# Performance work log

Measured on AMD Instinct MI355X. Metric: run time of the kernel, lower is better.

Reference implementation:

```python
import jax, jax.numpy as jnp
import numpy as np

B, TK, NK, H, E, V = 128, 400, 50, 256, 256, 50000


def setup_inputs() -> dict:
    key = jax.random.key(0)
    ks = iter(jax.random.split(key, 48))
    def rn(shape, s=1.0):
        return jax.random.normal(next(ks), shape, jnp.float32) * s
    def ru(shape):
        return jax.random.uniform(next(ks), shape, jnp.float32)
    z = lambda shape: jnp.zeros(shape, jnp.float32)
    s = 0.05
    inp = {}
    inp['y_t_1'] = jax.random.randint(next(ks), (B,), 0, V)
    inp['h_prev'] = rn((B, H))
    inp['c_prev'] = rn((B, H))
    inp['encoder_outputs'] = rn((B, TK, H))
    inp['encoder_outputs_node'] = rn((B, NK, H))
    inp['enc_padding_mask'] = jnp.ones((B, TK), jnp.float32)
    inp['enc_padding_mask_node'] = jnp.ones((B, NK), jnp.float32)
    inp['c_t_d'] = rn((B, H))
    inp['c_t_g'] = rn((B, H))
    inp['c_t_g2'] = rn((B, H))
    inp['coverage'] = z((B, TK))
    inp['flow'] = ru((B, NK))
    inp['node_to_token'] = ru((B, NK, TK))
    inp['graph'] = ru((B, NK, NK))
    inp['voc_d'] = jax.random.randint(next(ks), (B, TK), 0, V)
    inp['step'] = 0
    # learned parameters
    inp['emb_table'] = rn((V, E), s)
    inp['Wx'] = rn((4 * H, E), s); inp['bx'] = z((E,))
    inp['Wi'] = rn((E, 4 * H), s); inp['Wh'] = rn((H, 4 * H), s)
    inp['bi'] = z((4 * H,)); inp['bh'] = z((4 * H,))
    inp['Whd'] = rn((H, H), s); inp['Wsd'] = rn((2 * H, H), s)
    inp['wcd'] = rn((H,), s); inp['vd'] = rn((H,), s); inp['bd'] = z((H,))
    inp['Wn'] = rn((H, H), s); inp['Wsf'] = rn((2 * H, H), s)
    inp['vf'] = rn((H,), s); inp['bf'] = z((H,))
    inp['Wpg'] = rn((5 * H + E, 1), s); inp['bpg'] = z((1,))
    inp['W1'] = rn((4 * H, H), s); inp['b1'] = z((H,))
    inp['W2'] = rn((H, V), s); inp['b2'] = z((V,))
    return inp


def _forward(y_t_1, h_prev, c_prev, enc, enc_n, mask_t, mask_n, c_t_d, c_t_g, c_t_g2,
             coverage, flow, n2t, graph, voc_d, emb_table, Wx, bx, Wi, Wh, bi, bh,
             Whd, Wsd, wcd, vd, bd, Wn, Wsf, vf, bf, Wpg, bpg, W1, b1, W2, b2):
    sig, tanh = jax.nn.sigmoid, jnp.tanh
    y_emb = emb_table[y_t_1]                                   # [B,E]
    x = jnp.concatenate([c_t_d, c_t_g, c_t_g2, y_emb], 1) @ Wx + bx
    # single-step LSTM (torch gate order i,f,g,o)
    gates = x @ Wi + h_prev @ Wh + bi + bh
    gi, gf, gg, go = jnp.split(gates, 4, axis=1)
    c_new = sig(gf) * c_prev + sig(gi) * tanh(gg)
    h_new = sig(go) * tanh(c_new)
    s_hat = jnp.concatenate([h_new, c_new], 1)                 # [B,2H]
    # doc attention with coverage (Bahdanau)
    e = tanh(enc @ Whd + (s_hat @ Wsd)[:, None, :] + coverage[:, :, None] * wcd + bd) @ vd
    a = jax.nn.softmax(e, axis=1) * mask_t
    a = a / a.sum(1, keepdims=True)                            # [B,TK]
    c_d = jnp.einsum('bt,bth->bh', a, enc)
    coverage_next = coverage + a
    # event-graph node attention (flow-weighted, one-hop propagation)
    en = tanh(enc_n @ Wn + (s_hat @ Wsf)[:, None, :] + bf) @ vf
    an = jax.nn.softmax(en, axis=1) * mask_n
    an = an / an.sum(1, keepdims=True)
    an = an * flow
    an = an / an.sum(1, keepdims=True)                         # [B,NK]
    c_g = jnp.einsum('bn,bnh->bh', an, enc_n)
    an2 = jnp.einsum('bn,bnm->bm', an, graph) * mask_n
    an2 = an2 / an2.sum(1, keepdims=True)
    c_g2 = jnp.einsum('bn,bnh->bh', an2, enc_n)
    a_n2t = jnp.einsum('bn,bnt->bt', an, n2t)
    a_n2t = a_n2t / a_n2t.sum(1, keepdims=True)
    # flow update: per-node max of token attention restricted to node tokens
    flow_ = jnp.max(a[:, None, :] * n2t, axis=2)               # [B,NK]
    flow_next = flow_ / flow_.sum(1, keepdims=True)
    # pointer-generator gate
    p_gen = sig(jnp.concatenate([c_d, c_g, c_g2, s_hat, x], 1) @ Wpg + bpg)  # [B,1]
    out = jnp.concatenate([h_new, c_d, c_g, c_g2], 1) @ W1 + b1
    vocab_dist = jax.nn.softmax(out @ W2 + b2, axis=1)         # [B,V]
    attn_all = a / a.sum(1, keepdims=True)
    attn_ = (1.0 - p_gen) * attn_all
    vocab_ = p_gen * vocab_dist
    rows = jnp.arange(vocab_.shape[0])[:, None]
    final_dist = vocab_.at[rows, voc_d].add(attn_)             # scatter_add over vocab
    return (final_dist, (h_new, c_new), c_d, c_g, c_g2, a, a_n2t, p_gen,
            coverage_next, flow_next)


def reference(y_t_1, h_prev, c_prev, encoder_outputs, encoder_outputs_node,
              enc_padding_mask, enc_padding_mask_node, c_t_d, c_t_g, c_t_g2,
              coverage, flow, node_to_token, graph, voc_d, step,
              emb_table, Wx, bx, Wi, Wh, bi, bh, Whd, Wsd, wcd, vd, bd,
              Wn, Wsf, vf, bf, Wpg, bpg, W1, b1, W2, b2):
    return _forward(y_t_1, h_prev, c_prev, encoder_outputs, encoder_outputs_node,
                    enc_padding_mask, enc_padding_mask_node, c_t_d, c_t_g, c_t_g2,
                    coverage, flow, node_to_token, graph, voc_d, emb_table, Wx, bx,
                    Wi, Wh, bi, bh, Whd, Wsd, wcd, vd, bd, Wn, Wsf, vf, bf,
                    Wpg, bpg, W1, b1, W2, b2)
```

## Files before the change

kernel.cpp:

```cpp
#include <hip/hip_runtime.h>
#include <stdint.h>


typedef unsigned short u16;
typedef unsigned int   u32;

#define Bv  128
#define TKv 400
#define NKv 50
#define Hv  256
#define Vv  50000
#define VPAD 50176
#define NSv 16
#define CHUNKv 3136

typedef __attribute__((ext_vector_type(8))) short bf16x8;
typedef __attribute__((ext_vector_type(4))) float f32x4;

__device__ float g_x[32768];
__device__ float g_xp[4 * 32768];
__device__ float g_gates[131072];
__device__ float g_h[32768];
__device__ float g_c[32768];
__device__ float g_sdp[2 * 32768];
__device__ float g_sfp[2 * 32768];
__device__ float g_e[51200];
__device__ float g_en[6400];
__device__ float g_a[51200];
__device__ float g_cd[32768];
__device__ float g_cdp[8 * 32768];
__device__ float g_cg[32768];
__device__ float g_cg2[32768];
__device__ float g_pg[128];
__device__ float g_o1[32768];
__device__ float g_vred[Bv * NSv * 2];
__device__ float g_logits[6400000];
__device__ u16   g_Wdt[256 * 256];
__device__ u16   g_Wnt[256 * 256];
__device__ u16   g_W2t[(size_t)VPAD * 256];
__device__ u16   g_encb[(size_t)Bv * TKv * 256];
__device__ u16   g_encnb[(size_t)Bv * NKv * 256];

__device__ __forceinline__ float sigm(float x) { return 1.f / (1.f + expf(-x)); }

__device__ __forceinline__ u16 f2bf(float f) {
    u32 u = __float_as_uint(f);
    return (u16)((u + 0x7fffu + ((u >> 16) & 1u)) >> 16);
}

__device__ __forceinline__ bf16x8 cvt8(const float* __restrict__ p) {
    const float4 a = *(const float4*)p;
    const float4 b = *(const float4*)(p + 4);
    bf16x8 r;
    r[0] = (short)f2bf(a.x); r[1] = (short)f2bf(a.y);
    r[2] = (short)f2bf(a.z); r[3] = (short)f2bf(a.w);
    r[4] = (short)f2bf(b.x); r[5] = (short)f2bf(b.y);
    r[6] = (short)f2bf(b.z); r[7] = (short)f2bf(b.w);
    return r;
}

__device__ __forceinline__ float fast_tanh(float x) {
    x = fminf(fmaxf(x, -15.f), 15.f);
    float e = __expf(2.f * x);
    return (e - 1.f) / (e + 1.f);
}

__device__ __forceinline__ void ms_merge(float& m1, float& s1, float m2, float s2) {
    float M = fmaxf(m1, m2);
    s1 = s1 * expf(m1 - M) + s2 * expf(m2 - M);
    m1 = M;
}

__global__ __launch_bounds__(256) void k_cvt(
    const float* __restrict__ src, u16* __restrict__ dst, int n8)
{
    int i = blockIdx.x * 256 + threadIdx.x;
    const int stride = gridDim.x * 256;
    for (; i < n8; i += stride)
        *(bf16x8*)(dst + (size_t)i * 8) = cvt8(src + (size_t)i * 8);
}

__global__ __launch_bounds__(256) void k_tc(
    const float* __restrict__ src, u16* __restrict__ dst, int K, int N)
{
    __shared__ float tile[32][33];
    const int n0 = blockIdx.x * 32, k0 = blockIdx.y * 32;
    const int tx = threadIdx.x & 31, ty = threadIdx.x >> 5;
    #pragma unroll
    for (int i = 0; i < 32; i += 8) {
        int k = k0 + ty + i, n = n0 + tx;
        tile[ty + i][tx] = (n < N) ? src[(size_t)k * N + n] : 0.f;
    }
    __syncthreads();
    #pragma unroll
    for (int i = 0; i < 32; i += 8) {
        int n = n0 + ty + i, k = k0 + tx;
        dst[(size_t)n * K + k] = f2bf(tile[tx][ty + i]);
    }
}

__global__ __launch_bounds__(256) void k_x(
    const int* __restrict__ y,
    const float* __restrict__ ctd, const float* __restrict__ ctg,
    const float* __restrict__ ctg2, const float* __restrict__ emb,
    const float* __restrict__ Wx)
{
    const int b = blockIdx.x, ks = blockIdx.y, j = threadIdx.x;
    __shared__ float cs[256];
    float v;
    if      (ks == 0) v = ctd [b * 256 + j];
    else if (ks == 1) v = ctg [b * 256 + j];
    else if (ks == 2) v = ctg2[b * 256 + j];
    else              v = emb[(size_t)y[b] * 256 + j];
    cs[j] = v;
    __syncthreads();

    float acc = 0.f;
    const float* w = Wx + (size_t)(ks * 256) * 256 + j;
    #pragma unroll 8
    for (int k = 0; k < 256; k++) acc += cs[k] * w[(size_t)k * 256];
    g_xp[ks * 32768 + b * 256 + j] = acc;
}

__global__ __launch_bounds__(256) void k_gates(
    const float* __restrict__ h_prev,
    const float* __restrict__ Wi, const float* __restrict__ Wh,
    const float* __restrict__ bi, const float* __restrict__ bh,
    const float* __restrict__ bx)
{
    const int b = blockIdx.x, cc = blockIdx.y, j = threadIdx.x;
    __shared__ float xs[256], hs[256];

    float xv = bx[j] + g_xp[b * 256 + j] + g_xp[32768 + b * 256 + j]
             + g_xp[65536 + b * 256 + j] + g_xp[98304 + b * 256 + j];
    xs[j] = xv;
    if (cc == 0) g_x[b * 256 + j] = xv;
    hs[j] = h_prev[b * 256 + j];
    __syncthreads();

    const int col = cc * 256 + j;
    float acc = bi[col] + bh[col];
    const float* wi = Wi + col;
    const float* wh = Wh + col;
    #pragma unroll 8
    for (int k = 0; k < 256; k++)
        acc += xs[k] * wi[(size_t)k * 1024] + hs[k] * wh[(size_t)k * 1024];
    g_gates[b * 1024 + col] = acc;
}

__global__ __launch_bounds__(256) void k_cellsd(
    const float* __restrict__ c_prev,
    const float* __restrict__ Wsd, const float* __restrict__ Wsf,
    float* __restrict__ out_h, float* __restrict__ out_c)
{
    const int b = blockIdx.x, ks = blockIdx.y, j = threadIdx.x;
    __shared__ float sh[256];

    const float* gb = g_gates + b * 1024;
    float gi_ = gb[j], gf_ = gb[256 + j], gg_ = gb[512 + j], go_ = gb[768 + j];
    float cp = c_prev[b * 256 + j];
    float cn = sigm(gf_) * cp + sigm(gi_) * tanhf(gg_);
    float hn = sigm(go_) * tanhf(cn);
    if (ks == 0) {
        g_h[b * 256 + j] = hn;  g_c[b * 256 + j] = cn;
        out_h[b * 256 + j] = hn; out_c[b * 256 + j] = cn;
    }
    sh[j] = (ks == 0) ? hn : cn;
    __syncthreads();

    float asd = 0.f, asf = 0.f;
    const float* wd = Wsd + (size_t)(ks * 256) * 256 + j;
    const float* wf = Wsf + (size_t)(ks * 256) * 256 + j;
    #pragma unroll 8
    for (int k = 0; k < 256; k++) {
        float sv = sh[k];
        asd += sv * wd[(size_t)k * 256];
        asf += sv * wf[(size_t)k * 256];
    }
    g_sdp[ks * 32768 + b * 256 + j] = asd;
    g_sfp[ks * 32768 + b * 256 + j] = asf;
}

__global__ __launch_bounds__(256) void k_scores(
    const u16* __restrict__ srcb, int R,
    const u16* __restrict__ Wt,
    const float* __restrict__ addv0,
    const float* __restrict__ addv1,
    const float* __restrict__ abias,
    const float* __restrict__ cov,
    const float* __restrict__ wcw,
    const float* __restrict__ vv,
    float* __restrict__ eout)
{
    const int b = blockIdx.y, t0 = blockIdx.x * 32;
    const int tid = threadIdx.x;
    const int lane = tid & 63, wave = tid >> 6;
    const int nlow = lane & 15, quad = lane >> 4;

    const u16* brow = Wt + (size_t)(wave * 64 + nlow) * 256 + quad * 8;

    bool tval[2]; const u16* arow[2];
    #pragma unroll
    for (int mi = 0; mi < 2; mi++) {
        int trow = t0 + mi * 16 + nlow;
        tval[mi] = trow < R;
        arow[mi] = srcb + ((size_t)b * R + trow) * 256 + quad * 8;
    }

    const f32x4 zf = {0.f, 0.f, 0.f, 0.f};
    f32x4 acc[2][4];
    #pragma unroll
    for (int mi = 0; mi < 2; mi++)
        #pragma unroll
        for (int ni = 0; ni < 4; ni++) acc[mi][ni] = zf;

    for (int k0 = 0; k0 < 256; k0 += 32) {
        bf16x8 af[2], bf[4];
        #pragma unroll
        for (int mi = 0; mi < 2; mi++) {
            af[mi] = (bf16x8){0, 0, 0, 0, 0, 0, 0, 0};
            if (tval[mi]) af[mi] = *(const bf16x8*)(arow[mi] + k0);
        }
        #pragma unroll
        for (int ni = 0; ni < 4; ni++)
            bf[ni] = *(const bf16x8*)(brow + ni * 4096 + k0);
        #pragma unroll
        for (int mi = 0; mi < 2; mi++)
            #pragma unroll
            for (int ni = 0; ni < 4; ni++)
                acc[mi][ni] = __builtin_amdgcn_mfma_f32_16x16x32_bf16(
                    af[mi], bf[ni], acc[mi][ni], 0, 0, 0);
    }

    __shared__ float part[4][32];
    #pragma unroll
    for (int mi = 0; mi < 2; mi++) {
        float covt[4];
        #pragma unroll
        for (int r = 0; r < 4; r++) {
            int t = t0 + mi * 16 + quad * 4 + r;
            covt[r] = (cov && t < R) ? cov[b * R + t] : 0.f;
        }
        float s4[4] = {0.f, 0.f, 0.f, 0.f};
        #pragma unroll
        for (int ni = 0; ni < 4; ni++) {
            int col = wave * 64 + ni * 16 + nlow;
            float vvc = vv[col];
            float adc = addv0[b * 256 + col] + addv1[b * 256 + col] + abias[col];
            float wcc = wcw ? wcw[col] : 0.f;
            #pragma unroll
            for (int r = 0; r < 4; r++)
                s4[r] += vvc * fast_tanh(acc[mi][ni][r] + adc + covt[r] * wcc);
        }
        #pragma unroll
        for (int r = 0; r < 4; r++) {
            float s = s4[r];
            s += __shfl_xor(s, 1, 64);
            s += __shfl_xor(s, 2, 64);
            s += __shfl_xor(s, 4, 64);
            s += __shfl_xor(s, 8, 64);
            if (nlow == 0) part[wave][mi * 16 + quad * 4 + r] = s;
        }
    }
    __syncthreads();
    if (tid < 32) {
        int t = t0 + tid;
        if (t < R)
            eout[b * R + t] =
                part[0][tid] + part[1][tid] + part[2][tid] + part[3][tid];
    }
}

__global__ __launch_bounds__(256) void k_doc(
    const float* __restrict__ mask,
    const float* __restrict__ cov,
    float* __restrict__ out_a, float* __restrict__ out_cov)
{
    const int b = blockIdx.x, tid = threadIdx.x;
    __shared__ float red[256];

    float e0 = g_e[b * TKv + tid];
    float e1 = (tid + 256 < TKv) ? g_e[b * TKv + tid + 256] : -1e30f;

    float m = fmaxf(e0, e1);
    red[tid] = m; __syncthreads();
    for (int s = 128; s > 0; s >>= 1) { if (tid < s) red[tid] = fmaxf(red[tid], red[tid + s]); __syncthreads(); }
    m = red[0]; __syncthreads();

    float p0 = expf(e0 - m) * mask[b * TKv + tid];
    float p1 = (tid + 256 < TKv) ? expf(e1 - m) * mask[b * TKv + tid + 256] : 0.f;
    red[tid] = p0 + p1; __syncthreads();
    for (int s = 128; s > 0; s >>= 1) { if (tid < s) red[tid] += red[tid + s]; __syncthreads(); }
    float inv = 1.f / red[0];

    float a0 = p0 * inv;
    g_a[b * TKv + tid] = a0;
    out_a[b * TKv + tid] = a0;
    out_cov[b * TKv + tid] = cov[b * TKv + tid] + a0;
    if (tid + 256 < TKv) {
        float a1 = p1 * inv;
        g_a[b * TKv + tid + 256] = a1;
        out_a[b * TKv + tid + 256] = a1;
        out_cov[b * TKv + tid + 256] = cov[b * TKv + tid + 256] + a1;
    }
}

__global__ __launch_bounds__(256) void k_cd(const float* __restrict__ enc)
{
    const int b = blockIdx.x, ks = blockIdx.y, tid = threadIdx.x;
    __shared__ float as_[50];
    if (tid < 50) as_[tid] = g_a[b * TKv + ks * 50 + tid];
    __syncthreads();

    const float* eb = enc + ((size_t)b * TKv + ks * 50) * 256 + tid;
    float acc = 0.f;
    #pragma unroll 10
    for (int t = 0; t < 50; t++) acc += as_[t] * eb[(size_t)t * 256];
    g_cdp[ks * 32768 + b * 256 + tid] = acc;
}

__global__ __launch_bounds__(256) void k_flow(
    const float* __restrict__ n2t, float* __restrict__ out_flow)
{
    const int b = blockIdx.x, tid = threadIdx.x;
    __shared__ float as_[TKv];
    __shared__ float fl[NKv];
    __shared__ float red[256];

    for (int t = tid; t < TKv; t += 256) as_[t] = g_a[b * TKv + t];
    __syncthreads();

    const int nn = tid >> 2, sub = tid & 3;
    float mx = 0.f;
    if (nn < NKv) {
        const float* nb = n2t + ((size_t)b * NKv + nn) * TKv + sub * 100;
        const float* ab = as_ + sub * 100;
        #pragma unroll 4
        for (int t = 0; t < 100; t++) mx = fmaxf(mx, ab[t] * nb[t]);
    }
    mx = fmaxf(mx, __shfl_xor(mx, 1, 64));
    mx = fmaxf(mx, __shfl_xor(mx, 2, 64));
    if (sub == 0 && nn < NKv) fl[nn] = mx;
    __syncthreads();

    float fv = (tid < NKv) ? fl[tid] : 0.f;
    red[tid] = fv; __syncthreads();
    for (int s = 128; s > 0; s >>= 1) { if (tid < s) red[tid] += red[tid + s]; __syncthreads(); }
    float fs = red[0];
    if (tid < NKv) out_flow[b * NKv + tid] = fl[tid] / fs;
}

__global__ __launch_bounds__(256) void k_node1(
    const float* __restrict__ encn,
    const float* __restrict__ maskn,
    const float* __restrict__ flow,
    const float* __restrict__ graph,
    const float* __restrict__ n2t,
    const float* __restrict__ Wpg, const float* __restrict__ bpg,
    float* __restrict__ out_cd, float* __restrict__ out_cg,
    float* __restrict__ out_cg2, float* __restrict__ out_ant,
    float* __restrict__ out_pgen)
{
    const int b = blockIdx.x, tid = threadIdx.x;
    __shared__ float ans[NKv], an2s[NKv], red[256];

    float cd = 0.f;
    #pragma unroll
    for (int i = 0; i < 8; i++) cd += g_cdp[i * 32768 + b * 256 + tid];
    g_cd[b * 256 + tid] = cd;
    out_cd[b * 256 + tid] = cd;

    float v = (tid < NKv) ? g_en[b * NKv + tid] : -1e30f;
    red[tid] = v; __syncthreads();
    for (int s = 128; s > 0; s >>= 1) { if (tid < s) red[tid] = fmaxf(red[tid], red[tid + s]); __syncthreads(); }
    float m = red[0]; __syncthreads();

    float p = (tid < NKv) ? expf(v - m) * maskn[b * NKv + tid] : 0.f;
    red[tid] = p; __syncthreads();
    for (int s = 128; s > 0; s >>= 1) { if (tid < s) red[tid] += red[tid + s]; __syncthreads(); }
    float S = red[0]; __syncthreads();
    p = (tid < NKv) ? (p / S) * flow[b * NKv + tid] : 0.f;
    red[tid] = p; __syncthreads();
    for (int s = 128; s > 0; s >>= 1) { if (tid < s) red[tid] += red[tid + s]; __syncthreads(); }
    float S2 = red[0]; __syncthreads();
    if (tid < NKv) ans[tid] = p / S2;
    __syncthreads();

    float q = 0.f;
    if (tid < NKv) {
        const float* gb = graph + (size_t)b * NKv * NKv + tid;
        #pragma unroll
        for (int n = 0; n < NKv; n++) q += ans[n] * gb[n * NKv];
        q *= maskn[b * NKv + tid];
    }
    red[tid] = q; __syncthreads();
    for (int s = 128; s > 0; s >>= 1) { if (tid < s) red[tid] += red[tid + s]; __syncthreads(); }
    float S3 = red[0]; __syncthreads();
    if (tid < NKv) an2s[tid] = q / S3;
    __syncthreads();

    float cg = 0.f, cg2 = 0.f;
    {
        const float* enb = encn + (size_t)b * NKv * 256 + tid;
        #pragma unroll
        for (int n = 0; n < NKv; n++) {
            float e = enb[n * 256];
            cg  += ans[n]  * e;
            cg2 += an2s[n] * e;
        }
    }
    g_cg[b * 256 + tid] = cg;   out_cg[b * 256 + tid] = cg;
    g_cg2[b * 256 + tid] = cg2; out_cg2[b * 256 + tid] = cg2;

    float at0 = 0.f, at1 = 0.f;
    {
        const float* nb = n2t + (size_t)b * NKv * TKv;
        #pragma unroll
        for (int n = 0; n < NKv; n++) {
            float an = ans[n];
            at0 += an * nb[n * TKv + tid];
            if (tid + 256 < TKv) at1 += an * nb[n * TKv + tid + 256];
        }
    }
    float loc = at0 + ((tid + 256 < TKv) ? at1 : 0.f);
    red[tid] = loc; __syncthreads();
    for (int s = 128; s > 0; s >>= 1) { if (tid < s) red[tid] += red[tid + s]; __syncthreads(); }
    float S4 = red[0]; __syncthreads();
    out_ant[b * TKv + tid] = at0 / S4;
    if (tid + 256 < TKv) out_ant[b * TKv + tid + 256] = at1 / S4;

    float hvv = g_h[b * 256 + tid], cvv = g_c[b * 256 + tid];
    float xvv = g_x[b * 256 + tid];
    float part = cd  * Wpg[tid]        + cg  * Wpg[256 + tid]
               + cg2 * Wpg[512 + tid]  + hvv * Wpg[768 + tid]
               + cvv * Wpg[1024 + tid] + xvv * Wpg[1280 + tid];
    red[tid] = part; __syncthreads();
    for (int s = 128; s > 0; s >>= 1) { if (tid < s) red[tid] += red[tid + s]; __syncthreads(); }
    if (tid == 0) {
        float pg = sigm(red[0] + bpg[0]);
        g_pg[b] = pg; out_pgen[b] = pg;
    }
}

__global__ __launch_bounds__(256) void k_o1(
    const float* __restrict__ W1, const float* __restrict__ b1)
{
    const int b = blockIdx.x, cc = blockIdx.y, tid = threadIdx.x;
    __shared__ float cat[1024];
    __shared__ float red[256];

    cat[tid]       = g_h  [b * 256 + tid];
    cat[256 + tid] = g_cd [b * 256 + tid];
    cat[512 + tid] = g_cg [b * 256 + tid];
    cat[768 + tid] = g_cg2[b * 256 + tid];
    __syncthreads();

    const int lane = tid & 63, kq = tid >> 6;
    const int col = cc * 64 + lane;
    const float* w  = W1 + (size_t)(kq * 256) * 256 + col;
    const float* cs = cat + kq * 256;
    float acc = 0.f;
    #pragma unroll 8
    for (int k = 0; k < 256; k++) acc += cs[k] * w[(size_t)k * 256];
    red[tid] = acc; __syncthreads();

    if (tid < 64) {
        float o = b1[cc * 64 + tid]
                + red[tid] + red[64 + tid] + red[128 + tid] + red[192 + tid];
        g_o1[b * 256 + cc * 64 + tid] = o;
    }
}

__global__ __launch_bounds__(256) void k_logits(const float* __restrict__ b2)
{
    const int v0 = blockIdx.x * 64;
    const int tid = threadIdx.x;
    const int lane = tid & 63, wave = tid >> 6;
    const int nlow = lane & 15, quad = lane >> 4;

    const float* a0p = g_o1 + (wave * 32 + nlow) * 256 + quad * 8;
    const float* a1p = a0p + 16 * 256;
    const u16* bbase = g_W2t + (size_t)(v0 + nlow) * 256 + quad * 8;

    const f32x4 zf = {0.f, 0.f, 0.f, 0.f};
    f32x4 acc0[4], acc1[4];
    #pragma unroll
    for (int i = 0; i < 4; i++) { acc0[i] = zf; acc1[i] = zf; }

    for (int k0 = 0; k0 < 256; k0 += 32) {
        bf16x8 a0 = cvt8(a0p + k0);
        bf16x8 a1 = cvt8(a1p + k0);
        #pragma unroll
        for (int nt = 0; nt < 4; nt++) {
            bf16x8 bf = *(const bf16x8*)(bbase + (size_t)nt * 4096 + k0);
            acc0[nt] = __builtin_amdgcn_mfma_f32_16x16x32_bf16(a0, bf, acc0[nt], 0, 0, 0);
            acc1[nt] = __builtin_amdgcn_mfma_f32_16x16x32_bf16(a1, bf, acc1[nt], 0, 0, 0);
        }
    }

    #pragma unroll
    for (int nt = 0; nt < 4; nt++) {
        int v = v0 + nt * 16 + nlow;
        if (v < Vv) {
            float bb = b2[v];
            #pragma unroll
            for (int r = 0; r < 4; r++) {
                int row0 = wave * 32 + quad * 4 + r;
                g_logits[(size_t)row0 * Vv + v]        = acc0[nt][r] + bb;
                g_logits[(size_t)(row0 + 16) * Vv + v] = acc1[nt][r] + bb;
            }
        }
    }
}

__global__ __launch_bounds__(256) void k_vpart()
{
    const int b = blockIdx.x, ks = blockIdx.y, tid = threadIdx.x;
    __shared__ float rm[256], rs[256];

    const int base = ks * CHUNKv;
    const int end  = min(base + CHUNKv, Vv);
    const int n4   = (end - base) >> 2;
    const float4* L4 = (const float4*)(g_logits + (size_t)b * Vv + base);

    float m = -1e30f, s = 0.f;
    for (int i = tid; i < n4; i += 256) {
        float4 x = L4[i];
        float mx = fmaxf(fmaxf(x.x, x.y), fmaxf(x.z, x.w));
        if (mx > m) { s *= expf(m - mx); m = mx; }
        s += expf(x.x - m) + expf(x.y - m) + expf(x.z - m) + expf(x.w - m);
    }
    rm[tid] = m; rs[tid] = s; __syncthreads();
    for (int off = 128; off > 0; off >>= 1) {
        if (tid < off) {
            float m1 = rm[tid], s1 = rs[tid];
            ms_merge(m1, s1, rm[tid + off], rs[tid + off]);
            rm[tid] = m1; rs[tid] = s1;
        }
        __syncthreads();
    }
    if (tid == 0) {
        g_vred[(b * NSv + ks) * 2]     = rm[0];
        g_vred[(b * NSv + ks) * 2 + 1] = rs[0];
    }
}

__global__ __launch_bounds__(256) void k_vwrite(float* __restrict__ outF)
{
    const int b = blockIdx.x, ks = blockIdx.y, tid = threadIdx.x;

    float M = -1e30f, S = 0.f;
    #pragma unroll
    for (int i = 0; i < NSv; i++) {
        float mi = g_vred[(b * NSv + i) * 2];
        float si = g_vred[(b * NSv + i) * 2 + 1];
        ms_merge(M, S, mi, si);
    }
    const float inv = g_pg[b] / S;

    const int base = ks * CHUNKv;
    const int end  = min(base + CHUNKv, Vv);
    const int n4   = (end - base) >> 2;
    const float4* L4 = (const float4*)(g_logits + (size_t)b * Vv + base);
    float4* O4 = (float4*)(outF + (size_t)b * Vv + base);

    for (int i = tid; i < n4; i += 256) {
        float4 x = L4[i];
        float4 r;
        r.x = expf(x.x - M) * inv;
        r.y = expf(x.y - M) * inv;
        r.z = expf(x.z - M) * inv;
        r.w = expf(x.w - M) * inv;
        O4[i] = r;
    }
}

__global__ __launch_bounds__(256) void k_scatter(
    float* __restrict__ outF, const int* __restrict__ vocd)
{
    const int b = blockIdx.x, tid = threadIdx.x;
    float* Ob = outF + (size_t)b * Vv;
    const float omp = 1.f - g_pg[b];
    for (int t = tid; t < TKv; t += 256)
        atomicAdd(Ob + vocd[b * TKv + t], omp * g_a[b * TKv + t]);
}


extern "C" void kernel_launch(void* const* d_in, const int* in_sizes, int n_in,
                              void* d_out, int out_size, void* d_ws, size_t ws_size,
                              hipStream_t stream)
{
    (void)in_sizes; (void)n_in; (void)out_size; (void)d_ws; (void)ws_size;

    const int*   y      = (const int*)d_in[0];
    const float* h_prev = (const float*)d_in[1];
    const float* c_prev = (const float*)d_in[2];
    const float* enc    = (const float*)d_in[3];
    const float* encn   = (const float*)d_in[4];
    const float* mask   = (const float*)d_in[5];
    const float* maskn  = (const float*)d_in[6];
    const float* ctd    = (const float*)d_in[7];
    const float* ctg    = (const float*)d_in[8];
    const float* ctg2   = (const float*)d_in[9];
    const float* cov    = (const float*)d_in[10];
    const float* flow   = (const float*)d_in[11];
    const float* n2t    = (const float*)d_in[12];
    const float* graph  = (const float*)d_in[13];
    const int*   vocd   = (const int*)d_in[14];
    const float* emb    = (const float*)d_in[16];
    const float* Wx     = (const float*)d_in[17];
    const float* bx     = (const float*)d_in[18];
    const float* Wi     = (const float*)d_in[19];
    const float* Wh     = (const float*)d_in[20];
    const float* bi     = (const float*)d_in[21];
    const float* bh     = (const float*)d_in[22];
    const float* Whd    = (const float*)d_in[23];
    const float* Wsd    = (const float*)d_in[24];
    const float* wcdw   = (const float*)d_in[25];
    const float* vd     = (const float*)d_in[26];
    const float* bd     = (const float*)d_in[27];
    const float* Wn     = (const float*)d_in[28];
    const float* Wsf    = (const float*)d_in[29];
    const float* vf     = (const float*)d_in[30];
    const float* bfv    = (const float*)d_in[31];
    const float* Wpg    = (const float*)d_in[32];
    const float* bpg    = (const float*)d_in[33];
    const float* W1     = (const float*)d_in[34];
    const float* b1     = (const float*)d_in[35];
    const float* W2     = (const float*)d_in[36];
    const float* b2     = (const float*)d_in[37];

    float* o = (float*)d_out;
    float* o_final = o;
    float* o_h     = o + 6400000;
    float* o_c     = o + 6432768;
    float* o_cd    = o + 6465536;
    float* o_cg    = o + 6498304;
    float* o_cg2   = o + 6531072;
    float* o_a     = o + 6563840;
    float* o_ant   = o + 6615040;
    float* o_pg    = o + 6666240;
    float* o_cov   = o + 6666368;
    float* o_fl    = o + 6717568;

    float* g_e_p;   hipGetSymbolAddress((void**)&g_e_p,   HIP_SYMBOL(g_e));
    float* g_en_p;  hipGetSymbolAddress((void**)&g_en_p,  HIP_SYMBOL(g_en));
    float* g_sdp_p; hipGetSymbolAddress((void**)&g_sdp_p, HIP_SYMBOL(g_sdp));
    float* g_sfp_p; hipGetSymbolAddress((void**)&g_sfp_p, HIP_SYMBOL(g_sfp));
    u16*   g_Wdt_p; hipGetSymbolAddress((void**)&g_Wdt_p, HIP_SYMBOL(g_Wdt));
    u16*   g_Wnt_p; hipGetSymbolAddress((void**)&g_Wnt_p, HIP_SYMBOL(g_Wnt));
    u16*   g_W2t_p; hipGetSymbolAddress((void**)&g_W2t_p, HIP_SYMBOL(g_W2t));
    u16*   g_encb_p;  hipGetSymbolAddress((void**)&g_encb_p,  HIP_SYMBOL(g_encb));
    u16*   g_encnb_p; hipGetSymbolAddress((void**)&g_encnb_p, HIP_SYMBOL(g_encnb));

    k_tc<<<dim3(8, 8), dim3(256), 0, stream>>>(Whd, g_Wdt_p, 256, 256);
    k_tc<<<dim3(8, 8), dim3(256), 0, stream>>>(Wn,  g_Wnt_p, 256, 256);
    k_tc<<<dim3(VPAD / 32, 8), dim3(256), 0, stream>>>(W2, g_W2t_p, 256, Vv);

    k_cvt<<<dim3(2048), dim3(256), 0, stream>>>(enc,  g_encb_p,  Bv * TKv * 256 / 8);
    k_cvt<<<dim3(800),  dim3(256), 0, stream>>>(encn, g_encnb_p, Bv * NKv * 256 / 8);

    k_x<<<dim3(Bv, 4), dim3(256), 0, stream>>>(y, ctd, ctg, ctg2, emb, Wx);

    k_gates<<<dim3(Bv, 4), dim3(256), 0, stream>>>(h_prev, Wi, Wh, bi, bh, bx);

    k_cellsd<<<dim3(Bv, 2), dim3(256), 0, stream>>>(c_prev, Wsd, Wsf, o_h, o_c);

    k_scores<<<dim3(13, Bv), dim3(256), 0, stream>>>(
        g_encb_p, TKv, g_Wdt_p, g_sdp_p, g_sdp_p + 32768, bd, cov, wcdw, vd, g_e_p);

    k_scores<<<dim3(2, Bv), dim3(256), 0, stream>>>(
        g_encnb_p, NKv, g_Wnt_p, g_sfp_p, g_sfp_p + 32768, bfv,
        nullptr, nullptr, vf, g_en_p);

    k_doc<<<dim3(Bv), dim3(256), 0, stream>>>(mask, cov, o_a, o_cov);

    k_cd<<<dim3(Bv, 8), dim3(256), 0, stream>>>(enc);

    k_flow<<<dim3(Bv), dim3(256), 0, stream>>>(n2t, o_fl);

    k_node1<<<dim3(Bv), dim3(256), 0, stream>>>(
        encn, maskn, flow, graph, n2t, Wpg, bpg,
        o_cd, o_cg, o_cg2, o_ant, o_pg);

    k_o1<<<dim3(Bv, 4), dim3(256), 0, stream>>>(W1, b1);

    k_logits<<<dim3(VPAD / 64), dim3(256), 0, stream>>>(b2);

    k_vpart<<<dim3(Bv, NSv), dim3(256), 0, stream>>>();

    k_vwrite<<<dim3(Bv, NSv), dim3(256), 0, stream>>>(o_final);

    k_scatter<<<dim3(Bv), dim3(256), 0, stream>>>(o_final, vocd);
}
```

Baseline: 506.3 us.

## Retile attention score GEMM over flattened rows with LDS-staged weight column slices

The score kernels now treat the batch and time dimensions as one flat M dimension. Each block handles 128 rows and one 64-column slice of the transposed weight, which is staged in shared memory, and A-fragment loads are software-prefetched. Because column slices are split across blocks, each block writes a partial score per slice, and the softmax kernels sum the four partials. Separately, k_o1 writes a bf16 copy of its output so the logits GEMM loads bf16 directly instead of converting fp32 on every load.

```diff
diff --git a/kernel.cpp b/kernel.cpp
--- a/kernel.cpp
+++ b/kernel.cpp
@@ -13,6 +13,8 @@
 #define VPAD 50176
 #define NSv 16
 #define CHUNKv 3136
+#define MDOC (Bv * TKv)
+#define MNODE (Bv * NKv)
 
 typedef __attribute__((ext_vector_type(8))) short bf16x8;
 typedef __attribute__((ext_vector_type(4))) float f32x4;
@@ -24,8 +26,8 @@
 __device__ float g_c[32768];
 __device__ float g_sdp[2 * 32768];
 __device__ float g_sfp[2 * 32768];
-__device__ float g_e[51200];
-__device__ float g_en[6400];
+__device__ float g_ep[4 * MDOC];
+__device__ float g_enp[4 * MNODE];
 __device__ float g_a[51200];
 __device__ float g_cd[32768];
 __device__ float g_cdp[8 * 32768];
@@ -33,6 +35,7 @@
 __device__ float g_cg2[32768];
 __device__ float g_pg[128];
 __device__ float g_o1[32768];
+__device__ __attribute__((aligned(16))) u16 g_o1b[32768];
 __device__ float g_vred[Bv * NSv * 2];
 __device__ float g_logits[6400000];
 __device__ u16   g_Wdt[256 * 256];
@@ -181,8 +184,9 @@
     g_sfp[ks * 32768 + b * 256 + j] = asf;
 }
 
+template<int R>
 __global__ __launch_bounds__(256) void k_scores(
-    const u16* __restrict__ srcb, int R,
+    const u16* __restrict__ srcb,
     const u16* __restrict__ Wt,
     const float* __restrict__ addv0,
     const float* __restrict__ addv1,
@@ -190,22 +194,29 @@
     const float* __restrict__ cov,
     const float* __restrict__ wcw,
     const float* __restrict__ vv,
-    float* __restrict__ eout)
-{
-    const int b = blockIdx.y, t0 = blockIdx.x * 32;
+    float* __restrict__ eout, int Mtot)
+{
     const int tid = threadIdx.x;
-    const int lane = tid & 63, wave = tid >> 6;
+    const int lane = tid & 63, w = tid >> 6;
     const int nlow = lane & 15, quad = lane >> 4;
-
-    const u16* brow = Wt + (size_t)(wave * 64 + nlow) * 256 + quad * 8;
-
-    bool tval[2]; const u16* arow[2];
-    #pragma unroll
-    for (int mi = 0; mi < 2; mi++) {
-        int trow = t0 + mi * 16 + nlow;
-        tval[mi] = trow < R;
-        arow[mi] = srcb + ((size_t)b * R + trow) * 256 + quad * 8;
-    }
+    const int c0 = blockIdx.y * 64;
+
+    __shared__ u16 Bs[64][264];
+    {
+        const u16* wsrc = Wt + (size_t)c0 * 256;
+        #pragma unroll
+        for (int j = 0; j < 8; j++) {
+            int chunk = tid + j * 256;
+            int row = chunk >> 5, c16 = chunk & 31;
+            *(bf16x8*)(&Bs[row][c16 * 8]) =
+                *(const bf16x8*)(wsrc + row * 256 + c16 * 8);
+        }
+    }
+    __syncthreads();
+
+    const int rowbase = blockIdx.x * 128 + w * 32;
+    const u16* a0 = srcb + (size_t)(rowbase + nlow) * 256 + quad * 8;
+    const u16* a1 = a0 + 16 * 256;
 
     const f32x4 zf = {0.f, 0.f, 0.f, 0.f};
     f32x4 acc[2][4];
@@ -214,43 +225,45 @@
         #pragma unroll
         for (int ni = 0; ni < 4; ni++) acc[mi][ni] = zf;
 
+    bf16x8 af0 = *(const bf16x8*)(a0);
+    bf16x8 af1 = *(const bf16x8*)(a1);
     for (int k0 = 0; k0 < 256; k0 += 32) {
-        bf16x8 af[2], bf[4];
-        #pragma unroll
-        for (int mi = 0; mi < 2; mi++) {
-            af[mi] = (bf16x8){0, 0, 0, 0, 0, 0, 0, 0};
-            if (tval[mi]) af[mi] = *(const bf16x8*)(arow[mi] + k0);
-        }
+        const int kn = (k0 + 32) & 255;
+        bf16x8 nf0 = *(const bf16x8*)(a0 + kn);
+        bf16x8 nf1 = *(const bf16x8*)(a1 + kn);
+        bf16x8 bf[4];
         #pragma unroll
         for (int ni = 0; ni < 4; ni++)
-            bf[ni] = *(const bf16x8*)(brow + ni * 4096 + k0);
-        #pragma unroll
-        for (int mi = 0; mi < 2; mi++)
-            #pragma unroll
-            for (int ni = 0; ni < 4; ni++)
-                acc[mi][ni] = __builtin_amdgcn_mfma_f32_16x16x32_bf16(
-                    af[mi], bf[ni], acc[mi][ni], 0, 0, 0);
-    }
-
-    __shared__ float part[4][32];
+            bf[ni] = *(const bf16x8*)(&Bs[ni * 16 + nlow][k0 + quad * 8]);
+        #pragma unroll
+        for (int ni = 0; ni < 4; ni++) {
+            acc[0][ni] = __builtin_amdgcn_mfma_f32_16x16x32_bf16(af0, bf[ni], acc[0][ni], 0, 0, 0);
+            acc[1][ni] = __builtin_amdgcn_mfma_f32_16x16x32_bf16(af1, bf[ni], acc[1][ni], 0, 0, 0);
+        }
+        af0 = nf0; af1 = nf1;
+    }
+
     #pragma unroll
     for (int mi = 0; mi < 2; mi++) {
-        float covt[4];
+        float covt[4]; int bidx[4];
         #pragma unroll
         for (int r = 0; r < 4; r++) {
-            int t = t0 + mi * 16 + quad * 4 + r;
-            covt[r] = (cov && t < R) ? cov[b * R + t] : 0.f;
+            int row = rowbase + mi * 16 + quad * 4 + r;
+            covt[r] = cov ? cov[row] : 0.f;
+            bidx[r] = row / R;
         }
         float s4[4] = {0.f, 0.f, 0.f, 0.f};
         #pragma unroll
         for (int ni = 0; ni < 4; ni++) {
-            int col = wave * 64 + ni * 16 + nlow;
+            int col = c0 + ni * 16 + nlow;
             float vvc = vv[col];
-            float adc = addv0[b * 256 + col] + addv1[b * 256 + col] + abias[col];
+            float ab  = abias[col];
             float wcc = wcw ? wcw[col] : 0.f;
             #pragma unroll
-            for (int r = 0; r < 4; r++)
+            for (int r = 0; r < 4; r++) {
+                float adc = addv0[bidx[r] * 256 + col] + addv1[bidx[r] * 256 + col] + ab;
                 s4[r] += vvc * fast_tanh(acc[mi][ni][r] + adc + covt[r] * wcc);
+            }
         }
         #pragma unroll
         for (int r = 0; r < 4; r++) {
@@ -259,15 +272,10 @@
             s += __shfl_xor(s, 2, 64);
             s += __shfl_xor(s, 4, 64);
             s += __shfl_xor(s, 8, 64);
-            if (nlow == 0) part[wave][mi * 16 + quad * 4 + r] = s;
-        }
-    }
-    __syncthreads();
-    if (tid < 32) {
-        int t = t0 + tid;
-        if (t < R)
-            eout[b * R + t] =
-                part[0][tid] + part[1][tid] + part[2][tid] + part[3][tid];
+            int row = rowbase + mi * 16 + quad * 4 + r;
+            if (nlow == 0)
+                eout[(size_t)blockIdx.y * Mtot + row] = s;
+        }
     }
 }
 
@@ -279,8 +287,13 @@
     const int b = blockIdx.x, tid = threadIdx.x;
     __shared__ float red[256];
 
-    float e0 = g_e[b * TKv + tid];
-    float e1 = (tid + 256 < TKv) ? g_e[b * TKv + tid + 256] : -1e30f;
+    float e0 = 0.f, e1s = 0.f;
+    #pragma unroll
+    for (int ch = 0; ch < 4; ch++) {
+        e0 += g_ep[ch * MDOC + b * TKv + tid];
+        if (tid + 256 < TKv) e1s += g_ep[ch * MDOC + b * TKv + tid + 256];
+    }
+    float e1 = (tid + 256 < TKv) ? e1s : -1e30f;
 
     float m = fmaxf(e0, e1);
     red[tid] = m; __syncthreads();
@@ -370,7 +383,12 @@
     g_cd[b * 256 + tid] = cd;
     out_cd[b * 256 + tid] = cd;
 
-    float v = (tid < NKv) ? g_en[b * NKv + tid] : -1e30f;
+    float v = -1e30f;
+    if (tid < NKv) {
+        v = 0.f;
+        #pragma unroll
+        for (int ch = 0; ch < 4; ch++) v += g_enp[ch * MNODE + b * NKv + tid];
+    }
     red[tid] = v; __syncthreads();
     for (int s = 128; s > 0; s >>= 1) { if (tid < s) red[tid] = fmaxf(red[tid], red[tid + s]); __syncthreads(); }
     float m = red[0]; __syncthreads();
@@ -468,6 +486,7 @@
         float o = b1[cc * 64 + tid]
                 + red[tid] + red[64 + tid] + red[128 + tid] + red[192 + tid];
         g_o1[b * 256 + cc * 64 + tid] = o;
+        g_o1b[b * 256 + cc * 64 + tid] = f2bf(o);
     }
 }
 
@@ -478,8 +497,8 @@
     const int lane = tid & 63, wave = tid >> 6;
     const int nlow = lane & 15, quad = lane >> 4;
 
-    const float* a0p = g_o1 + (wave * 32 + nlow) * 256 + quad * 8;
-    const float* a1p = a0p + 16 * 256;
+    const u16* a0p = g_o1b + (wave * 32 + nlow) * 256 + quad * 8;
+    const u16* a1p = a0p + 16 * 256;
     const u16* bbase = g_W2t + (size_t)(v0 + nlow) * 256 + quad * 8;
 
     const f32x4 zf = {0.f, 0.f, 0.f, 0.f};
@@ -488,8 +507,8 @@
     for (int i = 0; i < 4; i++) { acc0[i] = zf; acc1[i] = zf; }
 
     for (int k0 = 0; k0 < 256; k0 += 32) {
-        bf16x8 a0 = cvt8(a0p + k0);
-        bf16x8 a1 = cvt8(a1p + k0);
+        bf16x8 a0 = *(const bf16x8*)(a0p + k0);
+        bf16x8 a1 = *(const bf16x8*)(a1p + k0);
         #pragma unroll
         for (int nt = 0; nt < 4; nt++) {
             bf16x8 bf = *(const bf16x8*)(bbase + (size_t)nt * 4096 + k0);
@@ -643,8 +662,8 @@
     float* o_cov   = o + 6666368;
     float* o_fl    = o + 6717568;
 
-    float* g_e_p;   hipGetSymbolAddress((void**)&g_e_p,   HIP_SYMBOL(g_e));
-    float* g_en_p;  hipGetSymbolAddress((void**)&g_en_p,  HIP_SYMBOL(g_en));
+    float* g_ep_p;  hipGetSymbolAddress((void**)&g_ep_p,  HIP_SYMBOL(g_ep));
+    float* g_enp_p; hipGetSymbolAddress((void**)&g_enp_p, HIP_SYMBOL(g_enp));
     float* g_sdp_p; hipGetSymbolAddress((void**)&g_sdp_p, HIP_SYMBOL(g_sdp));
     float* g_sfp_p; hipGetSymbolAddress((void**)&g_sfp_p, HIP_SYMBOL(g_sfp));
     u16*   g_Wdt_p; hipGetSymbolAddress((void**)&g_Wdt_p, HIP_SYMBOL(g_Wdt));
@@ -666,12 +685,13 @@
 
     k_cellsd<<<dim3(Bv, 2), dim3(256), 0, stream>>>(c_prev, Wsd, Wsf, o_h, o_c);
 
-    k_scores<<<dim3(13, Bv), dim3(256), 0, stream>>>(
-        g_encb_p, TKv, g_Wdt_p, g_sdp_p, g_sdp_p + 32768, bd, cov, wcdw, vd, g_e_p);
-
-    k_scores<<<dim3(2, Bv), dim3(256), 0, stream>>>(
-        g_encnb_p, NKv, g_Wnt_p, g_sfp_p, g_sfp_p + 32768, bfv,
-        nullptr, nullptr, vf, g_en_p);
+    k_scores<TKv><<<dim3(MDOC / 128, 4), dim3(256), 0, stream>>>(
+        g_encb_p, g_Wdt_p, g_sdp_p, g_sdp_p + 32768, bd, cov, wcdw, vd,
+        g_ep_p, MDOC);
+
+    k_scores<NKv><<<dim3(MNODE / 128, 4), dim3(256), 0, stream>>>(
+        g_encnb_p, g_Wnt_p, g_sfp_p, g_sfp_p + 32768, bfv,
+        nullptr, nullptr, vf, g_enp_p, MNODE);
 
     k_doc<<<dim3(Bv), dim3(256), 0, stream>>>(mask, cov, o_a, o_cov);
 
```

Result: faster. 481.6 us (-4.9%).
